# Kernel optimization log

Measured on AMD Instinct MI355X. Metric: run time of the kernel, lower is better.

The kernel has to match this reference:

```python
import jax, jax.numpy as jnp
import numpy as np

# ---- static config (matches init_kwargs) ----
N_NODES = 100_000; N_GRAPHS = 100; NPG = 1000; GRID = 32  # ceil(sqrt(1000))
N_EDGES = 1_600_000
IN_DIM = 64; POS_DIM = 16; HID = 16; HEADS = 4; HD = HID * HEADS  # 64
OUT_DIM = 10; DIV_WEIGHT = 0.1; BN_EPS = 1e-5; NEG_SLOPE = 0.2


def _segment_softmax(e, dst, n):
    emax = jax.ops.segment_max(e, dst, num_segments=n)
    p = jnp.exp(e - emax[dst])
    denom = jax.ops.segment_sum(p, dst, num_segments=n)
    return p / (denom[dst] + 1e-16)


def _gat(x, src, dst, n, W, a_src, a_dst, extra=None):
    """GATv1-style conv: per-head linear, additive attention, segment softmax over dst."""
    H, D = a_src.shape
    h = (x @ W).reshape(n, H, D)          # [N,H,D]
    s = (h * a_src).sum(-1)               # [N,H]
    d = (h * a_dst).sum(-1)               # [N,H]
    e = s[src] + d[dst]
    if extra is not None:
        e = e + extra                     # positional attention bias [E,H]
    e = jax.nn.leaky_relu(e, NEG_SLOPE)
    alpha = _segment_softmax(e, dst, n)   # [E,H]
    out = jax.ops.segment_sum(alpha[:, :, None] * h[src], dst, num_segments=n)
    return out.reshape(n, H * D)


def _div_loss(W):
    # head-diversity / orthogonality regularizer on per-head weight slices
    in_dim = W.shape[0]
    Wh = W.reshape(in_dim, HEADS, HID).transpose(1, 0, 2).reshape(HEADS, -1)
    Wn = Wh / (jnp.linalg.norm(Wh, axis=-1, keepdims=True) + 1e-12)
    G = Wn @ Wn.T
    off = G - jnp.eye(HEADS, dtype=W.dtype)
    return DIV_WEIGHT * (off ** 2).sum() / (HEADS * (HEADS - 1))


def _grid_pos(n, dtype):
    # normalized grid positions per graph (equal-size graphs of NPG nodes)
    i = jnp.arange(n) % NPG
    return jnp.stack([(i // GRID) / (GRID - 1), (i % GRID) / (GRID - 1)], -1).astype(dtype)


def _forward(x, edge_index, batch,
             pe_W, pe_b,
             l0_pW, l0_pas, l0_pad, l0_posW, l0_posb, l0_dW, l0_das, l0_dad, l0_fW, l0_fb, l0_g, l0_b,
             l1_pW, l1_pas, l1_pad, l1_posW, l1_posb, l1_dW, l1_das, l1_dad, l1_fW, l1_fb, l1_g, l1_b,
             res_W, res_b, task_W, task_b):
    n = x.shape[0]
    src, dst = edge_index[0], edge_index[1]
    pos = _grid_pos(n, x.dtype)
    rel = pos[dst] - pos[src]             # [E,2]
    h = jnp.concatenate([x, pos @ pe_W + pe_b], -1)  # positional encoding concat [N,80]

    def layer(h_in, pW, pas, pad, posW, posb, dW, das, dad, fW, fb, g, b):
        pos_out = _gat(h_in, src, dst, n, pW, pas, pad, extra=rel @ posW + posb)
        div_out = _gat(h_in, src, dst, n, dW, das, dad)
        fused = jnp.concatenate([pos_out, div_out], -1) @ fW + fb
        mu = fused.mean(0)
        var = fused.var(0)
        bn = (fused - mu) / jnp.sqrt(var + BN_EPS) * g + b
        return jax.nn.elu(bn), _div_loss(dW)

    h1, dl0 = layer(h, l0_pW, l0_pas, l0_pad, l0_posW, l0_posb, l0_dW, l0_das, l0_dad, l0_fW, l0_fb, l0_g, l0_b)
    h2, dl1 = layer(h1, l1_pW, l1_pas, l1_pad, l1_posW, l1_posb, l1_dW, l1_das, l1_dad, l1_fW, l1_fb, l1_g, l1_b)
    h2 = h2 + (h1 @ res_W + res_b)        # residual on layer >0

    pooled = jax.ops.segment_sum(h2, batch, num_segments=N_GRAPHS) / NPG  # mean pool
    task = pooled @ task_W + task_b       # [N_GRAPHS, OUT_DIM]
    return task, dl0 + dl1


def setup_inputs() -> dict:
    key = jax.random.key(0)
    keys = iter(jax.random.split(key, 64))
    nk = lambda: next(keys)
    w = lambda shape: jax.random.normal(nk(), shape, jnp.float32) * 0.05
    x = jax.random.normal(nk(), (N_NODES, IN_DIM), jnp.float32)
    gid = jnp.repeat(jnp.arange(N_GRAPHS), N_EDGES // N_GRAPHS)
    src = gid * NPG + jax.random.randint(nk(), (N_EDGES,), 0, NPG)
    dst = gid * NPG + jax.random.randint(nk(), (N_EDGES,), 0, NPG)
    edge_index = jnp.stack([src, dst]).astype(jnp.int32)
    batch = jnp.repeat(jnp.arange(N_GRAPHS), NPG).astype(jnp.int32)
    IN0 = IN_DIM + POS_DIM
    inp = dict(x=x, edge_index=edge_index, batch=batch,
               pe_W=w((2, POS_DIM)), pe_b=jnp.zeros((POS_DIM,), jnp.float32))
    for pref, din in (('l0', IN0), ('l1', HD)):
        inp[pref + '_pW'] = w((din, HD)); inp[pref + '_pas'] = w((HEADS, HID)); inp[pref + '_pad'] = w((HEADS, HID))
        inp[pref + '_posW'] = w((2, HEADS)); inp[pref + '_posb'] = jnp.zeros((HEADS,), jnp.float32)
        inp[pref + '_dW'] = w((din, HD)); inp[pref + '_das'] = w((HEADS, HID)); inp[pref + '_dad'] = w((HEADS, HID))
        inp[pref + '_fW'] = w((2 * HD, HD)); inp[pref + '_fb'] = jnp.zeros((HD,), jnp.float32)
        inp[pref + '_g'] = jnp.ones((HD,), jnp.float32); inp[pref + '_b'] = jnp.zeros((HD,), jnp.float32)
    inp['res_W'] = w((HD, HD)); inp['res_b'] = jnp.zeros((HD,), jnp.float32)
    inp['task_W'] = w((HD, OUT_DIM)); inp['task_b'] = jnp.zeros((OUT_DIM,), jnp.float32)
    return inp


def reference(x, edge_index, batch,
              pe_W, pe_b,
              l0_pW, l0_pas, l0_pad, l0_posW, l0_posb, l0_dW, l0_das, l0_dad, l0_fW, l0_fb, l0_g, l0_b,
              l1_pW, l1_pas, l1_pad, l1_posW, l1_posb, l1_dW, l1_das, l1_dad, l1_fW, l1_fb, l1_g, l1_b,
              res_W, res_b, task_W, task_b):
    return _forward(x, edge_index, batch, pe_W, pe_b,
                    l0_pW, l0_pas, l0_pad, l0_posW, l0_posb, l0_dW, l0_das, l0_dad, l0_fW, l0_fb, l0_g, l0_b,
                    l1_pW, l1_pas, l1_pad, l1_posW, l1_posb, l1_dW, l1_das, l1_dad, l1_fW, l1_fb, l1_g, l1_b,
                    res_W, res_b, task_W, task_b)
```

## Files before the change

### kernel.cpp

```cpp
#include <hip/hip_runtime.h>
#include <math.h>

#define N_NODES   100000
#define N_GRAPHS  100
#define NPG       1000
#define N_EDGES   1600000
#define EPG       16000
#define HID       16
#define HEADS     4
#define HD        64
#define OUT_DIM   10
#define BN_EPS    1e-5f
#define NEG_SLOPE 0.2f

#define LDA 68
#define BF_BLOCKS 782

static const size_t OFF_SPART = 0;
static const size_t OFF_PEWS  = 7000000;
static const size_t OFF_STAT1 = 7001000;
static const size_t OFF_WFRAG = 7010000;
static const size_t OFF_WF2   = 7020000;
static const size_t OFF_POOL  = 7100000;
static const size_t OFF_HL    = 8000000;
static const size_t OFF_CAT   = 20800000;
static const size_t OFF_F0    = 33600000;
static const size_t OFF_F1    = 40000000;
static const size_t OFF_SPSP  = 46400000;
static const size_t OFF_SPSD  = 46800000;
static const size_t OFF_DPD   = 47200000;
static const size_t OFF_STATS = 48000000;
static const size_t OFF_CSR   = 48000128;
static const size_t OFF_SRT   = 48100144;

__device__ inline unsigned bf_pack(float x, float y) {
    unsigned ux = __float_as_uint(x);
    unsigned uy = __float_as_uint(y);
    ux = (ux + 0x7FFFu + ((ux >> 16) & 1u)) >> 16;
    uy = ((uy + 0x7FFFu + ((uy >> 16) & 1u)) >> 16) << 16;
    return ux | uy;
}
__device__ inline float bf_lo(unsigned u) { return __uint_as_float(u << 16); }
__device__ inline float bf_hi(unsigned u) { return __uint_as_float(u & 0xFFFF0000u); }

typedef __attribute__((ext_vector_type(8))) short bf16x8;
typedef __attribute__((ext_vector_type(4))) float f32x4;

__device__ inline bf16x8 frag_from(unsigned a, unsigned b, unsigned c, unsigned d) {
    uint4 u{a, b, c, d};
    return *reinterpret_cast<bf16x8*>(&u);
}

__global__ __launch_bounds__(1024) void sort_edges(const int* __restrict__ ei,
                                                   int* __restrict__ csr_off,
                                                   int* __restrict__ sorted_src) {
    __shared__ int hist[1024];
    __shared__ int scan[1024];
    const int g = blockIdx.x;
    const int t = threadIdx.x;
    const int* src = ei;
    const int* dst = ei + N_EDGES;
    const int e0 = g * EPG;
    const int nbase = g * NPG;

    hist[t] = 0;
    __syncthreads();
    for (int i = t; i < EPG; i += 1024) {
        int d = dst[e0 + i] - nbase;
        atomicAdd(&hist[d], 1);
    }
    __syncthreads();
    scan[t] = hist[t];
    __syncthreads();
    for (int off = 1; off < 1024; off <<= 1) {
        int v = (t >= off) ? scan[t - off] : 0;
        __syncthreads();
        scan[t] += v;
        __syncthreads();
    }
    int excl = scan[t] - hist[t];
    if (t < NPG) csr_off[nbase + t] = e0 + excl;
    if (g == 0 && t == 0) csr_off[N_NODES] = N_EDGES;
    __syncthreads();
    hist[t] = excl;
    __syncthreads();
    for (int i = t; i < EPG; i += 1024) {
        int s = src[e0 + i];
        int d = dst[e0 + i] - nbase;
        int slot = atomicAdd(&hist[d], 1);
        sorted_src[e0 + slot] = s;
    }
}

__global__ __launch_bounds__(256) void prep_all(const float* __restrict__ peW, const float* __restrict__ peb,
                                                const float* __restrict__ pW0, const float* __restrict__ dW0,
                                                const float* __restrict__ pW1, const float* __restrict__ dW1,
                                                const float* __restrict__ fW0, const float* __restrict__ fW1,
                                                float* __restrict__ pe,
                                                uint4* __restrict__ wfA,
                                                uint4* __restrict__ wfD,
                                                float* __restrict__ pool2,
                                                float* __restrict__ stats0,
                                                float* __restrict__ stats1) {
    const int t = threadIdx.x;
    const int b = blockIdx.x;
    if (b == 0) {
        if (t < 128) {
            int r = t >> 6, c = t & 63;
            float sp = 0.f, sd = 0.f;
            for (int m = 0; m < 16; ++m) {
                sp += peW[r * 16 + m] * pW0[(64 + m) * 64 + c];
                sd += peW[r * 16 + m] * dW0[(64 + m) * 64 + c];
            }
            pe[r * 64 + c] = sp;
            pe[192 + r * 64 + c] = sd;
        } else if (t < 192) {
            int c = t & 63;
            float sp = 0.f, sd = 0.f;
            for (int m = 0; m < 16; ++m) {
                sp += peb[m] * pW0[(64 + m) * 64 + c];
                sd += peb[m] * dW0[(64 + m) * 64 + c];
            }
            pe[128 + c] = sp;
            pe[320 + c] = sd;
        }
    } else if (b == 1) {
        for (int i = t; i < 2 * 4 * 4 * 64; i += 256) {
            const int lane  = i & 63;
            const int ct    = (i >> 6) & 3;
            const int kk    = (i >> 8) & 3;
            const int layer = i >> 10;
            const float* W = layer ? fW1 : fW0;
            const int col = ct * 16 + (lane & 15);
            const int kb  = kk * 32 + (lane >> 4) * 8;
            uint4 u;
            u.x = bf_pack(W[(kb + 0) * 64 + col], W[(kb + 1) * 64 + col]);
            u.y = bf_pack(W[(kb + 2) * 64 + col], W[(kb + 3) * 64 + col]);
            u.z = bf_pack(W[(kb + 4) * 64 + col], W[(kb + 5) * 64 + col]);
            u.w = bf_pack(W[(kb + 6) * 64 + col], W[(kb + 7) * 64 + col]);
            wfA[i] = u;
        }
    } else if (b == 2) {
        for (int i = t; i < 2048; i += 256) {
            const int lane  = i & 63;
            const int ct    = (i >> 6) & 3;
            const int kk    = (i >> 8) & 1;
            const int mat   = (i >> 9) & 1;
            const int layer = i >> 10;
            const float* W = layer ? (mat ? dW1 : pW1) : (mat ? dW0 : pW0);
            const int col = ct * 16 + (lane & 15);
            const int kb  = kk * 32 + (lane >> 4) * 8;
            uint4 u;
            u.x = bf_pack(W[(kb + 0) * 64 + col], W[(kb + 1) * 64 + col]);
            u.y = bf_pack(W[(kb + 2) * 64 + col], W[(kb + 3) * 64 + col]);
            u.z = bf_pack(W[(kb + 4) * 64 + col], W[(kb + 5) * 64 + col]);
            u.w = bf_pack(W[(kb + 6) * 64 + col], W[(kb + 7) * 64 + col]);
            wfD[i] = u;
        }
    } else {
        for (int i = t; i < 2 * N_GRAPHS * 64; i += 256) pool2[i] = 0.f;
        if (t < 128) { stats0[t] = 0.f; stats1[t] = 0.f; }
    }
}

__global__ __launch_bounds__(128) void reduce_stats(const float* __restrict__ part,
                                                    float* __restrict__ stats, int nb) {
    const int c = threadIdx.x;
    const int per = (nb + gridDim.x - 1) / gridDim.x;
    const int b0 = blockIdx.x * per;
    int b1 = b0 + per; if (b1 > nb) b1 = nb;
    float s = 0.f;
    for (int b = b0; b < b1; ++b) s += part[(size_t)b * 128 + c];
    atomicAdd(&stats[c], s);
}

template <bool PE, bool BN>
__global__ __launch_bounds__(256) void gemm_dual_mfma(const float* __restrict__ A,
                                                      const unsigned* __restrict__ wf2,
                                                      const float* __restrict__ pe,
                                                      const float* __restrict__ pas,
                                                      const float* __restrict__ pad_,
                                                      const float* __restrict__ das,
                                                      const float* __restrict__ dad,
                                                      const float* __restrict__ posW,
                                                      const float* __restrict__ posb,
                                                      const float* __restrict__ stats,
                                                      const float* __restrict__ gamma,
                                                      const float* __restrict__ beta,
                                                      float* __restrict__ poolF,
                                                      unsigned* __restrict__ hl,
                                                      float* __restrict__ sps_p,
                                                      float* __restrict__ sps_d,
                                                      float2* __restrict__ dpd) {
    __shared__ float sD[4 * 2 * 16 * LDA];
    const int t = threadIdx.x;
    const int w = t >> 6, lane = t & 63;
    const int cidx = lane & 15, khi = lane >> 4;
    const int node0 = blockIdx.x * 64;

    bf16x8 wf[2][2][4];
#pragma unroll
    for (int mat = 0; mat < 2; ++mat)
#pragma unroll
        for (int kk = 0; kk < 2; ++kk)
#pragma unroll
            for (int ct = 0; ct < 4; ++ct)
                wf[mat][kk][ct] = *reinterpret_cast<const bf16x8*>(
                    wf2 + (size_t)((((mat * 2 + kk) * 4 + ct) * 64) + lane) * 4);

    const int node0w = node0 + w * 16;
    int gn = node0w + cidx; if (gn > N_NODES - 1) gn = N_NODES - 1;
    const float* ar = A + (size_t)gn * 64;
    bf16x8 ah[2], al[2];
#pragma unroll
    for (int kk = 0; kk < 2; ++kk) {
        const int k0 = kk * 32 + khi * 8;
        float4 f0 = *reinterpret_cast<const float4*>(ar + k0);
        float4 f1 = *reinterpret_cast<const float4*>(ar + k0 + 4);
        if (BN) {
            const float invN = 1.0f / (float)N_NODES;
            float4 sa = *reinterpret_cast<const float4*>(&stats[k0]);
            float4 sb = *reinterpret_cast<const float4*>(&stats[k0 + 4]);
            float4 qa = *reinterpret_cast<const float4*>(&stats[64 + k0]);
            float4 qb = *reinterpret_cast<const float4*>(&stats[64 + k0 + 4]);
            float4 ga = *reinterpret_cast<const float4*>(&gamma[k0]);
            float4 gb = *reinterpret_cast<const float4*>(&gamma[k0 + 4]);
            float4 ba = *reinterpret_cast<const float4*>(&beta[k0]);
            float4 bb = *reinterpret_cast<const float4*>(&beta[k0 + 4]);
            float sc[8], sh[8];
            float ss[8] = {sa.x, sa.y, sa.z, sa.w, sb.x, sb.y, sb.z, sb.w};
            float qq[8] = {qa.x, qa.y, qa.z, qa.w, qb.x, qb.y, qb.z, qb.w};
            float gg[8] = {ga.x, ga.y, ga.z, ga.w, gb.x, gb.y, gb.z, gb.w};
            float bt[8] = {ba.x, ba.y, ba.z, ba.w, bb.x, bb.y, bb.z, bb.w};
#pragma unroll
            for (int i = 0; i < 8; ++i) {
                float mu = ss[i] * invN;
                float var = qq[i] * invN - mu * mu;
                float iv = rsqrtf(var + BN_EPS);
                sc[i] = iv * gg[i];
                sh[i] = bt[i] - mu * sc[i];
            }
            auto ap = [&](float v, int i) {
                float r = fmaf(v, sc[i], sh[i]);
                return r > 0.f ? r : (__expf(r) - 1.f);
            };
            f0.x = ap(f0.x, 0); f0.y = ap(f0.y, 1); f0.z = ap(f0.z, 2); f0.w = ap(f0.w, 3);
            f1.x = ap(f1.x, 4); f1.y = ap(f1.y, 5); f1.z = ap(f1.z, 6); f1.w = ap(f1.w, 7);
            if (node0w < N_NODES) {
                const int node_l = node0w + cidx;
                const bool okn = node_l < N_NODES;
                const int gl = node_l / NPG;
                const int g0 = node0w / NPG;
                int lastn = node0w + 15; if (lastn > N_NODES - 1) lastn = N_NODES - 1;
                const int g1 = lastn / NPG;
                float p8[8] = {f0.x, f0.y, f0.z, f0.w, f1.x, f1.y, f1.z, f1.w};
                {
                    const bool m = okn && (gl == g0);
#pragma unroll
                    for (int i = 0; i < 8; ++i) {
                        float tv = m ? p8[i] : 0.f;
                        tv += __shfl_xor(tv, 1); tv += __shfl_xor(tv, 2);
                        tv += __shfl_xor(tv, 4); tv += __shfl_xor(tv, 8);
                        if (cidx == 0) atomicAdd(&poolF[g0 * 64 + k0 + i], tv);
                    }
                }
                if (g1 != g0) {
                    const bool m = okn && (gl == g1);
#pragma unroll
                    for (int i = 0; i < 8; ++i) {
                        float tv = m ? p8[i] : 0.f;
                        tv += __shfl_xor(tv, 1); tv += __shfl_xor(tv, 2);
                        tv += __shfl_xor(tv, 4); tv += __shfl_xor(tv, 8);
                        if (cidx == 0) atomicAdd(&poolF[g1 * 64 + k0 + i], tv);
                    }
                }
            }
        }
        unsigned h0 = bf_pack(f0.x, f0.y), h1 = bf_pack(f0.z, f0.w);
        unsigned h2 = bf_pack(f1.x, f1.y), h3 = bf_pack(f1.z, f1.w);
        unsigned l0 = bf_pack(f0.x - bf_lo(h0), f0.y - bf_hi(h0));
        unsigned l1 = bf_pack(f0.z - bf_lo(h1), f0.w - bf_hi(h1));
        unsigned l2 = bf_pack(f1.x - bf_lo(h2), f1.y - bf_hi(h2));
        unsigned l3 = bf_pack(f1.z - bf_lo(h3), f1.w - bf_hi(h3));
        ah[kk] = frag_from(h0, h1, h2, h3);
        al[kk] = frag_from(l0, l1, l2, l3);
    }

    f32x4 ap4[4], ad4[4];
#pragma unroll
    for (int ct = 0; ct < 4; ++ct) { ap4[ct] = 0.f; ad4[ct] = 0.f; }
#pragma unroll
    for (int ct = 0; ct < 4; ++ct) {
        ap4[ct] = __builtin_amdgcn_mfma_f32_16x16x32_bf16(ah[0], wf[0][0][ct], ap4[ct], 0, 0, 0);
        ap4[ct] = __builtin_amdgcn_mfma_f32_16x16x32_bf16(ah[1], wf[0][1][ct], ap4[ct], 0, 0, 0);
        ap4[ct] = __builtin_amdgcn_mfma_f32_16x16x32_bf16(al[0], wf[0][0][ct], ap4[ct], 0, 0, 0);
        ap4[ct] = __builtin_amdgcn_mfma_f32_16x16x32_bf16(al[1], wf[0][1][ct], ap4[ct], 0, 0, 0);
        ad4[ct] = __builtin_amdgcn_mfma_f32_16x16x32_bf16(ah[0], wf[1][0][ct], ad4[ct], 0, 0, 0);
        ad4[ct] = __builtin_amdgcn_mfma_f32_16x16x32_bf16(ah[1], wf[1][1][ct], ad4[ct], 0, 0, 0);
        ad4[ct] = __builtin_amdgcn_mfma_f32_16x16x32_bf16(al[0], wf[1][0][ct], ad4[ct], 0, 0, 0);
        ad4[ct] = __builtin_amdgcn_mfma_f32_16x16x32_bf16(al[1], wf[1][1][ct], ad4[ct], 0, 0, 0);
    }

    {
        float* base = sD + w * (2 * 16 * LDA);
#pragma unroll
        for (int ct = 0; ct < 4; ++ct)
#pragma unroll
            for (int q = 0; q < 4; ++q) {
                base[(khi * 4 + q) * LDA + ct * 16 + cidx]                 = ap4[ct][q];
                base[16 * LDA + (khi * 4 + q) * LDA + ct * 16 + cidx]      = ad4[ct][q];
            }
    }
    __syncthreads();

    const int tx = t & 15, ty = t >> 4;
    const int c4 = tx * 4;
    float4 accp[4], accd[4];
#pragma unroll
    for (int j = 0; j < 4; ++j) {
        const int n = ty * 4 + j;
        const float* bp = sD + (n >> 4) * (2 * 16 * LDA) + (n & 15) * LDA;
        accp[j] = *reinterpret_cast<const float4*>(bp + c4);
        accd[j] = *reinterpret_cast<const float4*>(bp + 16 * LDA + c4);
    }

    if (PE) {
        float4 pp0 = *reinterpret_cast<const float4*>(&pe[c4]);
        float4 pp1 = *reinterpret_cast<const float4*>(&pe[64 + c4]);
        float4 ppb = *reinterpret_cast<const float4*>(&pe[128 + c4]);
        float4 pd0 = *reinterpret_cast<const float4*>(&pe[192 + c4]);
        float4 pd1 = *reinterpret_cast<const float4*>(&pe[256 + c4]);
        float4 pdb = *reinterpret_cast<const float4*>(&pe[320 + c4]);
#pragma unroll
        for (int j = 0; j < 4; ++j) {
            int node = node0 + ty * 4 + j;
            int r = node % NPG;
            float px = (float)(r >> 5) * (1.0f / 31.0f);
            float py = (float)(r & 31) * (1.0f / 31.0f);
            accp[j].x += px * pp0.x + py * pp1.x + ppb.x;
            accp[j].y += px * pp0.y + py * pp1.y + ppb.y;
            accp[j].z += px * pp0.z + py * pp1.z + ppb.z;
            accp[j].w += px * pp0.w + py * pp1.w + ppb.w;
            accd[j].x += px * pd0.x + py * pd1.x + pdb.x;
            accd[j].y += px * pd0.y + py * pd1.y + pdb.y;
            accd[j].z += px * pd0.z + py * pd1.z + pdb.z;
            accd[j].w += px * pd0.w + py * pd1.w + pdb.w;
        }
    }

    float4 pasv = *reinterpret_cast<const float4*>(&pas[c4]);
    float4 padv = *reinterpret_cast<const float4*>(&pad_[c4]);
    float4 dasv = *reinterpret_cast<const float4*>(&das[c4]);
    float4 dadv = *reinterpret_cast<const float4*>(&dad[c4]);
    const int h = tx >> 2;
    const float pw0 = posW[h], pw1 = posW[4 + h], pb = posb[h];
    const int cu = tx * 2;
#pragma unroll
    for (int j = 0; j < 4; ++j) {
        const int node = node0 + ty * 4 + j;
        float vps = accp[j].x * pasv.x + accp[j].y * pasv.y + accp[j].z * pasv.z + accp[j].w * pasv.w;
        float vpd = accp[j].x * padv.x + accp[j].y * padv.y + accp[j].z * padv.z + accp[j].w * padv.w;
        float vds = accd[j].x * dasv.x + accd[j].y * dasv.y + accd[j].z * dasv.z + accd[j].w * dasv.w;
        float vdd = accd[j].x * dadv.x + accd[j].y * dadv.y + accd[j].z * dadv.z + accd[j].w * dadv.w;
        vps += __shfl_xor(vps, 1); vps += __shfl_xor(vps, 2);
        vpd += __shfl_xor(vpd, 1); vpd += __shfl_xor(vpd, 2);
        vds += __shfl_xor(vds, 1); vds += __shfl_xor(vds, 2);
        vdd += __shfl_xor(vdd, 1); vdd += __shfl_xor(vdd, 2);
        if (node < N_NODES) {
            uint2 up, ud;
            up.x = bf_pack(accp[j].x, accp[j].y); up.y = bf_pack(accp[j].z, accp[j].w);
            ud.x = bf_pack(accd[j].x, accd[j].y); ud.y = bf_pack(accd[j].z, accd[j].w);
            *reinterpret_cast<uint2*>(&hl[(size_t)node * 64 + cu])      = up;
            *reinterpret_cast<uint2*>(&hl[(size_t)node * 64 + 32 + cu]) = ud;
            if ((tx & 3) == 0) {
                const int r = node % NPG;
                const float pxn = (float)(r >> 5) * (1.0f / 31.0f);
                const float pyn = (float)(r & 31) * (1.0f / 31.0f);
                const float posdot = pxn * pw0 + pyn * pw1;
                sps_p[node * 4 + h] = vps - posdot;
                sps_d[node * 4 + h] = vds;
                dpd[node * 4 + h] = float2{vpd + posdot + pb, vdd};
            }
        }
    }
}

__global__ __launch_bounds__(256) void gemm_mfma_bf(const unsigned* __restrict__ A,
                                                    const unsigned* __restrict__ wfrag,
                                                    const float* __restrict__ bias,
                                                    float* __restrict__ out,
                                                    float* __restrict__ spart) {
    __shared__ float red[512];
    const int t = threadIdx.x;
    const int lane = t & 63;
    const int cidx = lane & 15;
    const int khi  = lane >> 4;

    bf16x8 wf[4][4];
#pragma unroll
    for (int kk = 0; kk < 4; ++kk)
#pragma unroll
        for (int ct = 0; ct < 4; ++ct)
            wf[kk][ct] = *reinterpret_cast<const bf16x8*>(wfrag + (size_t)((kk * 4 + ct) * 64 + lane) * 4);

    float bias_r[4];
#pragma unroll
    for (int ct = 0; ct < 4; ++ct) bias_r[ct] = bias[ct * 16 + cidx];

    float ls[4] = {0.f, 0.f, 0.f, 0.f};
    float lq[4] = {0.f, 0.f, 0.f, 0.f};

    const int NW  = gridDim.x << 2;
    const int wid = (blockIdx.x << 2) + (t >> 6);
    for (int tile = wid; tile < N_NODES / 16; tile += NW) {
        const int node0 = tile << 4;
        const unsigned* arow = A + (size_t)(node0 + cidx) * 64 + khi * 4;
        bf16x8 a0 = *reinterpret_cast<const bf16x8*>(arow);
        bf16x8 a1 = *reinterpret_cast<const bf16x8*>(arow + 16);
        bf16x8 a2 = *reinterpret_cast<const bf16x8*>(arow + 32);
        bf16x8 a3 = *reinterpret_cast<const bf16x8*>(arow + 48);

        f32x4 acc[4];
#pragma unroll
        for (int ct = 0; ct < 4; ++ct) acc[ct] = 0.f;
#pragma unroll
        for (int ct = 0; ct < 4; ++ct) {
            acc[ct] = __builtin_amdgcn_mfma_f32_16x16x32_bf16(a0, wf[0][ct], acc[ct], 0, 0, 0);
            acc[ct] = __builtin_amdgcn_mfma_f32_16x16x32_bf16(a1, wf[1][ct], acc[ct], 0, 0, 0);
            acc[ct] = __builtin_amdgcn_mfma_f32_16x16x32_bf16(a2, wf[2][ct], acc[ct], 0, 0, 0);
            acc[ct] = __builtin_amdgcn_mfma_f32_16x16x32_bf16(a3, wf[3][ct], acc[ct], 0, 0, 0);
        }

        const int nbase = node0 + (khi << 2);
#pragma unroll
        for (int ct = 0; ct < 4; ++ct) {
#pragma unroll
            for (int q = 0; q < 4; ++q) {
                float v = acc[ct][q] + bias_r[ct];
                out[(size_t)(nbase + q) * 64 + ct * 16 + cidx] = v;
                ls[ct] += v;
                lq[ct] = fmaf(v, v, lq[ct]);
            }
        }
    }

#pragma unroll
    for (int ct = 0; ct < 4; ++ct) {
        ls[ct] += __shfl_xor(ls[ct], 16); ls[ct] += __shfl_xor(ls[ct], 32);
        lq[ct] += __shfl_xor(lq[ct], 16); lq[ct] += __shfl_xor(lq[ct], 32);
    }
    if (lane < 16) {
        const int w = t >> 6;
#pragma unroll
        for (int ct = 0; ct < 4; ++ct) {
            red[w * 64 + ct * 16 + lane]       = ls[ct];
            red[256 + w * 64 + ct * 16 + lane] = lq[ct];
        }
    }
    __syncthreads();
    if (t < 64) {
        float s  = red[t] + red[64 + t] + red[128 + t] + red[192 + t];
        float sq = red[256 + t] + red[320 + t] + red[384 + t] + red[448 + t];
        spart[(size_t)blockIdx.x * 128 + t]      = s;
        spart[(size_t)blockIdx.x * 128 + 64 + t] = sq;
    }
}

__global__ __launch_bounds__(256) void gat_fused(const unsigned* __restrict__ hl,
                                                 const float* __restrict__ sps_p,
                                                 const float* __restrict__ sps_d,
                                                 const float2* __restrict__ dpd,
                                                 const int* __restrict__ csr_off,
                                                 const int* __restrict__ sorted_src,
                                                 unsigned* __restrict__ gat_cat) {
    const int b = blockIdx.x;
    const int logical = (b & 7) * 3125 + (b >> 3);
    const int v = logical * 4 + (threadIdx.x >> 6);
    if (v >= N_NODES) return;
    const int lane = threadIdx.x & 63;
    const int j1 = lane >> 3;
    const int p1 = (lane >> 2) & 1;
    const int h1 = lane & 3;
    const int phneed = ((lane >> 5) << 2) | ((lane & 31) >> 3);

    const float* __restrict__ spl = p1 ? sps_d : sps_p;
    const float2 dv1 = dpd[(size_t)v * 4 + h1];
    const float dval1 = p1 ? dv1.y : dv1.x;

    const int beg = __builtin_amdgcn_readfirstlane(csr_off[v]);
    const int end = __builtin_amdgcn_readfirstlane(csr_off[v + 1]);

    float2 acc = {0.f, 0.f};
    float wpart = 0.f;
    int e = beg;
    const int nfull = (end - beg) >> 3;

    int sA = 0, sB = 0;
    float svA = 0.f, svB = 0.f;
    if (nfull >= 1) { sA = sorted_src[e + j1]; svA = spl[(size_t)sA * 4 + h1]; }
    if (nfull >= 2) { sB = sorted_src[e + 8 + j1]; }

    for (int k = 0; k < nfull; ++k, e += 8) {
        int sC = 0;
        if (k + 2 < nfull) sC = sorted_src[e + 16 + j1];
        if (k + 1 < nfull) svB = spl[(size_t)sB * 4 + h1];
        float elog = svA + dval1;
        elog = fmaxf(elog, NEG_SLOPE * elog);
        float w = __expf(elog);
        wpart += w;
#pragma unroll
        for (int jj = 0; jj < 8; ++jj) {
            int sj = __builtin_amdgcn_readlane(sA, jj * 8);
            float wj = __shfl(w, jj * 8 + phneed);
            unsigned u = hl[((size_t)sj << 6) + lane];
            acc.x = fmaf(wj, bf_lo(u), acc.x);
            acc.y = fmaf(wj, bf_hi(u), acc.y);
        }
        sA = sB; sB = sC; svA = svB;
    }

    if (e < end) {
        const int nj = end - e;
        int ee = e + j1; if (ee >= end) ee = end - 1;
        int s = sorted_src[ee];
        float sval = spl[(size_t)s * 4 + h1];
        float elog = sval + dval1;
        elog = fmaxf(elog, NEG_SLOPE * elog);
        float w = __expf(elog);
        if (j1 >= nj) w = 0.f;
        wpart += w;
        for (int jj = 0; jj < nj; ++jj) {
            int sj = __builtin_amdgcn_readlane(s, jj * 8);
            float wj = __shfl(w, jj * 8 + phneed);
            unsigned u = hl[((size_t)sj << 6) + lane];
            acc.x = fmaf(wj, bf_lo(u), acc.x);
            acc.y = fmaf(wj, bf_hi(u), acc.y);
        }
    }
    wpart += __shfl_xor(wpart, 8);
    wpart += __shfl_xor(wpart, 16);
    wpart += __shfl_xor(wpart, 32);
    const float wsum = __shfl(wpart, phneed);
    const float inv = 1.0f / (wsum + 1e-16f);
    gat_cat[(size_t)v * 64 + lane] = bf_pack(acc.x * inv, acc.y * inv);
}

template <bool WRITEF>
__global__ __launch_bounds__(256) void bn_elu(float* __restrict__ F, const float* __restrict__ stats,
                                              const float* __restrict__ gamma, const float* __restrict__ beta,
                                              float* __restrict__ pooled) {
    __shared__ float red[256];
    const int t = threadIdx.x;
    const int idx = blockIdx.x * 256 + t;
    const int c = t & 63;
    float mu = stats[c] * (1.0f / (float)N_NODES);
    float var = stats[64 + c] * (1.0f / (float)N_NODES) - mu * mu;
    float inv = rsqrtf(var + BN_EPS);
    float v = (F[idx] - mu) * inv * gamma[c] + beta[c];
    v = (v > 0.f) ? v : expm1f(v);
    if (WRITEF) F[idx] = v;
    red[t] = v;
    __syncthreads();
    if (t < 64) {
        float s = red[c] + red[64 + c] + red[128 + c] + red[192 + c];
        int g = (blockIdx.x * 4) / NPG;
        atomicAdd(&pooled[g * 64 + c], s);
    }
}

__global__ __launch_bounds__(64) void task_head(const float* __restrict__ pooled,
                                                const float* __restrict__ pooledF0,
                                                const float* __restrict__ resW,
                                                const float* __restrict__ resb,
                                                const float* __restrict__ taskW,
                                                const float* __restrict__ taskb,
                                                float* __restrict__ out) {
    const int g = blockIdx.x;
    const int c = threadIdx.x;
    float rc = 0.f;
    const float* pf = pooledF0 + g * 64;
    for (int k = 0; k < 64; ++k)
        rc = fmaf(pf[k], resW[k * 64 + c], rc);
    float p = (pooled[g * 64 + c] + rc) * (1.0f / (float)NPG) + resb[c];
#pragma unroll
    for (int o = 0; o < OUT_DIM; ++o) {
        float partial = p * taskW[c * OUT_DIM + o];
#pragma unroll
        for (int m = 1; m < 64; m <<= 1) partial += __shfl_xor(partial, m);
        if (c == 0) out[g * OUT_DIM + o] = partial + taskb[o];
    }
}

__global__ __launch_bounds__(256) void div_loss(const float* __restrict__ dW0,
                                                const float* __restrict__ dW1,
                                                float* __restrict__ out) {
    __shared__ float red[16][16];
    float total = 0.f;
    for (int layer = 0; layer < 2; ++layer) {
        const float* W = layer ? dW1 : dW0;
        const int din = layer ? 64 : 80;
        const int p = threadIdx.x & 15;
        const int s16 = threadIdx.x >> 4;
        const int i = p >> 2, j = p & 3;
        float acc = 0.f;
        const int Kk = din * 16;
        for (int kk = s16; kk < Kk; kk += 16) {
            int rrow = kk >> 4, cc = kk & 15;
            acc += W[rrow * 64 + i * 16 + cc] * W[rrow * 64 + j * 16 + cc];
        }
        red[p][s16] = acc;
        __syncthreads();
        if (threadIdx.x < 16) {
            float s = 0.f;
            for (int m = 0; m < 16; ++m) s += red[threadIdx.x][m];
            red[threadIdx.x][0] = s;
        }
        __syncthreads();
        if (threadIdx.x == 0) {
            float G[4][4], nrm[4];
            for (int a = 0; a < 4; ++a)
                for (int b = 0; b < 4; ++b) G[a][b] = red[a * 4 + b][0];
            for (int a = 0; a < 4; ++a) nrm[a] = sqrtf(G[a][a]) + 1e-12f;
            float l = 0.f;
            for (int a = 0; a < 4; ++a)
                for (int b = 0; b < 4; ++b) {
                    float gn = G[a][b] / (nrm[a] * nrm[b]);
                    float off = gn - (a == b ? 1.f : 0.f);
                    l += off * off;
                }
            total += 0.1f * l / 12.f;
        }
        __syncthreads();
    }
    if (threadIdx.x == 0) *out = total;
}

extern "C" void kernel_launch(void* const* d_in, const int* in_sizes, int n_in,
                              void* d_out, int out_size, void* d_ws, size_t ws_size,
                              hipStream_t stream) {
    const float* x      = (const float*)d_in[0];
    const int*   ei     = (const int*)d_in[1];
    const float* peW    = (const float*)d_in[3];
    const float* peb    = (const float*)d_in[4];

    const float* l_pW[2]   = {(const float*)d_in[5],  (const float*)d_in[17]};
    const float* l_pas[2]  = {(const float*)d_in[6],  (const float*)d_in[18]};
    const float* l_pad[2]  = {(const float*)d_in[7],  (const float*)d_in[19]};
    const float* l_posW[2] = {(const float*)d_in[8],  (const float*)d_in[20]};
    const float* l_posb[2] = {(const float*)d_in[9],  (const float*)d_in[21]};
    const float* l_dW[2]   = {(const float*)d_in[10], (const float*)d_in[22]};
    const float* l_das[2]  = {(const float*)d_in[11], (const float*)d_in[23]};
    const float* l_dad[2]  = {(const float*)d_in[12], (const float*)d_in[24]};
    const float* l_fW[2]   = {(const float*)d_in[13], (const float*)d_in[25]};
    const float* l_fb[2]   = {(const float*)d_in[14], (const float*)d_in[26]};
    const float* l_g[2]    = {(const float*)d_in[15], (const float*)d_in[27]};
    const float* l_b[2]    = {(const float*)d_in[16], (const float*)d_in[28]};
    const float* res_W  = (const float*)d_in[29];
    const float* res_b  = (const float*)d_in[30];
    const float* task_W = (const float*)d_in[31];
    const float* task_b = (const float*)d_in[32];

    float* ws = (float*)d_ws;
    float* spart   = ws + OFF_SPART;
    float* pe_ws   = ws + OFF_PEWS;
    float* stats1  = ws + OFF_STAT1;
    float* wfrag   = ws + OFF_WFRAG;
    float* wfrag2  = ws + OFF_WF2;
    float* pooled  = ws + OFF_POOL;
    float* pooledF0= ws + OFF_POOL + 6400;
    unsigned* hl   = (unsigned*)(ws + OFF_HL);
    unsigned* cat_bf = (unsigned*)(ws + OFF_CAT);
    float* F0      = ws + OFF_F0;
    float* F1      = ws + OFF_F1;
    float* sps_p   = ws + OFF_SPSP;
    float* sps_d   = ws + OFF_SPSD;
    float2* dpd    = (float2*)(ws + OFF_DPD);
    float* stats0  = ws + OFF_STATS;
    int*   csr_off    = (int*)(ws + OFF_CSR);
    int*   sorted_src = (int*)(ws + OFF_SRT);
    float* out = (float*)d_out;

    const int NODE_BLOCKS = (N_NODES + 3) / 4;
    const int GEMM_BLOCKS = (N_NODES + 63) / 64;
    const int BN_BLOCKS   = N_NODES * 64 / 256;

    sort_edges<<<N_GRAPHS, 1024, 0, stream>>>(ei, csr_off, sorted_src);
    prep_all<<<4, 256, 0, stream>>>(peW, peb, l_pW[0], l_dW[0], l_pW[1], l_dW[1],
                                    l_fW[0], l_fW[1], pe_ws,
                                    (uint4*)wfrag, (uint4*)wfrag2,
                                    pooled, stats0, stats1);

    gemm_dual_mfma<true, false><<<GEMM_BLOCKS, 256, 0, stream>>>(x, (const unsigned*)wfrag2, pe_ws,
        l_pas[0], l_pad[0], l_das[0], l_dad[0], l_posW[0], l_posb[0],
        stats0, l_g[0], l_b[0], pooledF0,
        hl, sps_p, sps_d, dpd);
    gat_fused<<<NODE_BLOCKS, 256, 0, stream>>>(hl, sps_p, sps_d, dpd, csr_off, sorted_src, cat_bf);
    gemm_mfma_bf<<<BF_BLOCKS, 256, 0, stream>>>(cat_bf, (const unsigned*)wfrag,
                                                l_fb[0], F0, spart);
    reduce_stats<<<16, 128, 0, stream>>>(spart, stats0, BF_BLOCKS);

    gemm_dual_mfma<false, true><<<GEMM_BLOCKS, 256, 0, stream>>>(F0, (const unsigned*)wfrag2 + 4096, pe_ws,
        l_pas[1], l_pad[1], l_das[1], l_dad[1], l_posW[1], l_posb[1],
        stats0, l_g[0], l_b[0], pooledF0,
        hl, sps_p, sps_d, dpd);
    gat_fused<<<NODE_BLOCKS, 256, 0, stream>>>(hl, sps_p, sps_d, dpd, csr_off, sorted_src, cat_bf);
    gemm_mfma_bf<<<BF_BLOCKS, 256, 0, stream>>>(cat_bf, (const unsigned*)wfrag + 4096,
                                                l_fb[1], F1, spart);
    reduce_stats<<<16, 128, 0, stream>>>(spart, stats1, BF_BLOCKS);
    bn_elu<false><<<BN_BLOCKS, 256, 0, stream>>>(F1, stats1, l_g[1], l_b[1], pooled);

    task_head<<<N_GRAPHS, 64, 0, stream>>>(pooled, pooledF0, res_W, res_b,
                                           task_W, task_b, out);
    div_loss<<<1, 256, 0, stream>>>(l_dW[0], l_dW[1], out + 1000);
}
```

Before: 457.3 us.

## Merge sort and prep kernels, batch gather loads, pool BN per graph chunk

Merges the edge-sort and weight-prep launches into one kernel that uses extra blocks for the prep work, removing one launch. The GAT aggregation loop is unrolled by hand so all eight neighbor-row gathers are issued before the FMAs, which raises memory-level parallelism. The final BN+ELU+pool kernel changes from 25,000 tiny blocks each doing one atomic to 500 blocks that each reduce 200 nodes, cutting atomic and launch overhead. In exchange, each pooling block does more serial work and there is less parallelism.

```diff
diff --git a/kernel.cpp b/kernel.cpp
--- a/kernel.cpp
+++ b/kernel.cpp
@@ -15,6 +15,8 @@
 
 #define LDA 68
 #define BF_BLOCKS 782
+#define PB_PER_GRAPH 5
+#define PB_NODES 200
 
 static const size_t OFF_SPART = 0;
 static const size_t OFF_PEWS  = 7000000;
@@ -51,13 +53,87 @@
     return *reinterpret_cast<bf16x8*>(&u);
 }
 
-__global__ __launch_bounds__(1024) void sort_edges(const int* __restrict__ ei,
-                                                   int* __restrict__ csr_off,
-                                                   int* __restrict__ sorted_src) {
+__global__ __launch_bounds__(1024) void sort_prep(const int* __restrict__ ei,
+                                                  int* __restrict__ csr_off,
+                                                  int* __restrict__ sorted_src,
+                                                  const float* __restrict__ peW, const float* __restrict__ peb,
+                                                  const float* __restrict__ pW0, const float* __restrict__ dW0,
+                                                  const float* __restrict__ pW1, const float* __restrict__ dW1,
+                                                  const float* __restrict__ fW0, const float* __restrict__ fW1,
+                                                  float* __restrict__ pe,
+                                                  uint4* __restrict__ wfA,
+                                                  uint4* __restrict__ wfD,
+                                                  float* __restrict__ pool2,
+                                                  float* __restrict__ stats0,
+                                                  float* __restrict__ stats1) {
+    const int g = blockIdx.x;
+    const int t = threadIdx.x;
+    if (g >= N_GRAPHS) {
+        const int b = g - N_GRAPHS;
+        if (b == 0) {
+            if (t < 128) {
+                int r = t >> 6, c = t & 63;
+                float sp = 0.f, sd = 0.f;
+                for (int m = 0; m < 16; ++m) {
+                    sp += peW[r * 16 + m] * pW0[(64 + m) * 64 + c];
+                    sd += peW[r * 16 + m] * dW0[(64 + m) * 64 + c];
+                }
+                pe[r * 64 + c] = sp;
+                pe[192 + r * 64 + c] = sd;
+            } else if (t < 192) {
+                int c = t & 63;
+                float sp = 0.f, sd = 0.f;
+                for (int m = 0; m < 16; ++m) {
+                    sp += peb[m] * pW0[(64 + m) * 64 + c];
+                    sd += peb[m] * dW0[(64 + m) * 64 + c];
+                }
+                pe[128 + c] = sp;
+                pe[320 + c] = sd;
+            }
+        } else if (b == 1) {
+            if (t < 256)
+            for (int i = t; i < 2 * 4 * 4 * 64; i += 256) {
+                const int lane  = i & 63;
+                const int ct    = (i >> 6) & 3;
+                const int kk    = (i >> 8) & 3;
+                const int layer = i >> 10;
+                const float* W = layer ? fW1 : fW0;
+                const int col = ct * 16 + (lane & 15);
+                const int kb  = kk * 32 + (lane >> 4) * 8;
+                uint4 u;
+                u.x = bf_pack(W[(kb + 0) * 64 + col], W[(kb + 1) * 64 + col]);
+                u.y = bf_pack(W[(kb + 2) * 64 + col], W[(kb + 3) * 64 + col]);
+                u.z = bf_pack(W[(kb + 4) * 64 + col], W[(kb + 5) * 64 + col]);
+                u.w = bf_pack(W[(kb + 6) * 64 + col], W[(kb + 7) * 64 + col]);
+                wfA[i] = u;
+            }
+        } else if (b == 2) {
+            if (t < 256)
+            for (int i = t; i < 2048; i += 256) {
+                const int lane  = i & 63;
+                const int ct    = (i >> 6) & 3;
+                const int kk    = (i >> 8) & 1;
+                const int mat   = (i >> 9) & 1;
+                const int layer = i >> 10;
+                const float* W = layer ? (mat ? dW1 : pW1) : (mat ? dW0 : pW0);
+                const int col = ct * 16 + (lane & 15);
+                const int kb  = kk * 32 + (lane >> 4) * 8;
+                uint4 u;
+                u.x = bf_pack(W[(kb + 0) * 64 + col], W[(kb + 1) * 64 + col]);
+                u.y = bf_pack(W[(kb + 2) * 64 + col], W[(kb + 3) * 64 + col]);
+                u.z = bf_pack(W[(kb + 4) * 64 + col], W[(kb + 5) * 64 + col]);
+                u.w = bf_pack(W[(kb + 6) * 64 + col], W[(kb + 7) * 64 + col]);
+                wfD[i] = u;
+            }
+        } else {
+            for (int i = t; i < 2 * N_GRAPHS * 64; i += 1024) pool2[i] = 0.f;
+            if (t < 128) { stats0[t] = 0.f; stats1[t] = 0.f; }
+        }
+        return;
+    }
+
     __shared__ int hist[1024];
     __shared__ int scan[1024];
-    const int g = blockIdx.x;
-    const int t = threadIdx.x;
     const int* src = ei;
     const int* dst = ei + N_EDGES;
     const int e0 = g * EPG;
@@ -89,77 +165,6 @@
         int d = dst[e0 + i] - nbase;
         int slot = atomicAdd(&hist[d], 1);
         sorted_src[e0 + slot] = s;
-    }
-}
-
-__global__ __launch_bounds__(256) void prep_all(const float* __restrict__ peW, const float* __restrict__ peb,
-                                                const float* __restrict__ pW0, const float* __restrict__ dW0,
-                                                const float* __restrict__ pW1, const float* __restrict__ dW1,
-                                                const float* __restrict__ fW0, const float* __restrict__ fW1,
-                                                float* __restrict__ pe,
-                                                uint4* __restrict__ wfA,
-                                                uint4* __restrict__ wfD,
-                                                float* __restrict__ pool2,
-                                                float* __restrict__ stats0,
-                                                float* __restrict__ stats1) {
-    const int t = threadIdx.x;
-    const int b = blockIdx.x;
-    if (b == 0) {
-        if (t < 128) {
-            int r = t >> 6, c = t & 63;
-            float sp = 0.f, sd = 0.f;
-            for (int m = 0; m < 16; ++m) {
-                sp += peW[r * 16 + m] * pW0[(64 + m) * 64 + c];
-                sd += peW[r * 16 + m] * dW0[(64 + m) * 64 + c];
-            }
-            pe[r * 64 + c] = sp;
-            pe[192 + r * 64 + c] = sd;
-        } else if (t < 192) {
-            int c = t & 63;
-            float sp = 0.f, sd = 0.f;
-            for (int m = 0; m < 16; ++m) {
-                sp += peb[m] * pW0[(64 + m) * 64 + c];
-                sd += peb[m] * dW0[(64 + m) * 64 + c];
-            }
-            pe[128 + c] = sp;
-            pe[320 + c] = sd;
-        }
-    } else if (b == 1) {
-        for (int i = t; i < 2 * 4 * 4 * 64; i += 256) {
-            const int lane  = i & 63;
-            const int ct    = (i >> 6) & 3;
-            const int kk    = (i >> 8) & 3;
-            const int layer = i >> 10;
-            const float* W = layer ? fW1 : fW0;
-            const int col = ct * 16 + (lane & 15);
-            const int kb  = kk * 32 + (lane >> 4) * 8;
-            uint4 u;
-            u.x = bf_pack(W[(kb + 0) * 64 + col], W[(kb + 1) * 64 + col]);
-            u.y = bf_pack(W[(kb + 2) * 64 + col], W[(kb + 3) * 64 + col]);
-            u.z = bf_pack(W[(kb + 4) * 64 + col], W[(kb + 5) * 64 + col]);
-            u.w = bf_pack(W[(kb + 6) * 64 + col], W[(kb + 7) * 64 + col]);
-            wfA[i] = u;
-        }
-    } else if (b == 2) {
-        for (int i = t; i < 2048; i += 256) {
-            const int lane  = i & 63;
-            const int ct    = (i >> 6) & 3;
-            const int kk    = (i >> 8) & 1;
-            const int mat   = (i >> 9) & 1;
-            const int layer = i >> 10;
-            const float* W = layer ? (mat ? dW1 : pW1) : (mat ? dW0 : pW0);
-            const int col = ct * 16 + (lane & 15);
-            const int kb  = kk * 32 + (lane >> 4) * 8;
-            uint4 u;
-            u.x = bf_pack(W[(kb + 0) * 64 + col], W[(kb + 1) * 64 + col]);
-            u.y = bf_pack(W[(kb + 2) * 64 + col], W[(kb + 3) * 64 + col]);
-            u.z = bf_pack(W[(kb + 4) * 64 + col], W[(kb + 5) * 64 + col]);
-            u.w = bf_pack(W[(kb + 6) * 64 + col], W[(kb + 7) * 64 + col]);
-            wfD[i] = u;
-        }
-    } else {
-        for (int i = t; i < 2 * N_GRAPHS * 64; i += 256) pool2[i] = 0.f;
-        if (t < 128) { stats0[t] = 0.f; stats1[t] = 0.f; }
     }
 }
 
@@ -508,14 +513,38 @@
         elog = fmaxf(elog, NEG_SLOPE * elog);
         float w = __expf(elog);
         wpart += w;
-#pragma unroll
-        for (int jj = 0; jj < 8; ++jj) {
-            int sj = __builtin_amdgcn_readlane(sA, jj * 8);
-            float wj = __shfl(w, jj * 8 + phneed);
-            unsigned u = hl[((size_t)sj << 6) + lane];
-            acc.x = fmaf(wj, bf_lo(u), acc.x);
-            acc.y = fmaf(wj, bf_hi(u), acc.y);
-        }
+        int sj0 = __builtin_amdgcn_readlane(sA, 0);
+        int sj1 = __builtin_amdgcn_readlane(sA, 8);
+        int sj2 = __builtin_amdgcn_readlane(sA, 16);
+        int sj3 = __builtin_amdgcn_readlane(sA, 24);
+        int sj4 = __builtin_amdgcn_readlane(sA, 32);
+        int sj5 = __builtin_amdgcn_readlane(sA, 40);
+        int sj6 = __builtin_amdgcn_readlane(sA, 48);
+        int sj7 = __builtin_amdgcn_readlane(sA, 56);
+        float wj0 = __shfl(w, 0 + phneed);
+        float wj1 = __shfl(w, 8 + phneed);
+        float wj2 = __shfl(w, 16 + phneed);
+        float wj3 = __shfl(w, 24 + phneed);
+        float wj4 = __shfl(w, 32 + phneed);
+        float wj5 = __shfl(w, 40 + phneed);
+        float wj6 = __shfl(w, 48 + phneed);
+        float wj7 = __shfl(w, 56 + phneed);
+        unsigned u0 = hl[((size_t)sj0 << 6) + lane];
+        unsigned u1 = hl[((size_t)sj1 << 6) + lane];
+        unsigned u2 = hl[((size_t)sj2 << 6) + lane];
+        unsigned u3 = hl[((size_t)sj3 << 6) + lane];
+        unsigned u4 = hl[((size_t)sj4 << 6) + lane];
+        unsigned u5 = hl[((size_t)sj5 << 6) + lane];
+        unsigned u6 = hl[((size_t)sj6 << 6) + lane];
+        unsigned u7 = hl[((size_t)sj7 << 6) + lane];
+        acc.x = fmaf(wj0, bf_lo(u0), acc.x); acc.y = fmaf(wj0, bf_hi(u0), acc.y);
+        acc.x = fmaf(wj1, bf_lo(u1), acc.x); acc.y = fmaf(wj1, bf_hi(u1), acc.y);
+        acc.x = fmaf(wj2, bf_lo(u2), acc.x); acc.y = fmaf(wj2, bf_hi(u2), acc.y);
+        acc.x = fmaf(wj3, bf_lo(u3), acc.x); acc.y = fmaf(wj3, bf_hi(u3), acc.y);
+        acc.x = fmaf(wj4, bf_lo(u4), acc.x); acc.y = fmaf(wj4, bf_hi(u4), acc.y);
+        acc.x = fmaf(wj5, bf_lo(u5), acc.x); acc.y = fmaf(wj5, bf_hi(u5), acc.y);
+        acc.x = fmaf(wj6, bf_lo(u6), acc.x); acc.y = fmaf(wj6, bf_hi(u6), acc.y);
+        acc.x = fmaf(wj7, bf_lo(u7), acc.x); acc.y = fmaf(wj7, bf_hi(u7), acc.y);
         sA = sB; sB = sC; svA = svB;
     }
 
@@ -545,27 +574,30 @@
     gat_cat[(size_t)v * 64 + lane] = bf_pack(acc.x * inv, acc.y * inv);
 }
 
-template <bool WRITEF>
-__global__ __launch_bounds__(256) void bn_elu(float* __restrict__ F, const float* __restrict__ stats,
-                                              const float* __restrict__ gamma, const float* __restrict__ beta,
-                                              float* __restrict__ pooled) {
+__global__ __launch_bounds__(256) void pool_bn(const float* __restrict__ F, const float* __restrict__ stats,
+                                               const float* __restrict__ gamma, const float* __restrict__ beta,
+                                               float* __restrict__ pooled) {
     __shared__ float red[256];
+    const int b = blockIdx.x;
+    const int g = b / PB_PER_GRAPH;
+    const int n0 = g * NPG + (b % PB_PER_GRAPH) * PB_NODES;
     const int t = threadIdx.x;
-    const int idx = blockIdx.x * 256 + t;
-    const int c = t & 63;
-    float mu = stats[c] * (1.0f / (float)N_NODES);
-    float var = stats[64 + c] * (1.0f / (float)N_NODES) - mu * mu;
-    float inv = rsqrtf(var + BN_EPS);
-    float v = (F[idx] - mu) * inv * gamma[c] + beta[c];
-    v = (v > 0.f) ? v : expm1f(v);
-    if (WRITEF) F[idx] = v;
-    red[t] = v;
+    const int c = t & 63, rg = t >> 6;
+    const float mu = stats[c] * (1.0f / (float)N_NODES);
+    const float var = stats[64 + c] * (1.0f / (float)N_NODES) - mu * mu;
+    const float iv = rsqrtf(var + BN_EPS);
+    const float sc = iv * gamma[c];
+    const float sh = beta[c] - mu * sc;
+    float s = 0.f;
+    for (int i = rg; i < PB_NODES; i += 4) {
+        float v = fmaf(F[(size_t)(n0 + i) * 64 + c], sc, sh);
+        v = (v > 0.f) ? v : expm1f(v);
+        s += v;
+    }
+    red[t] = s;
     __syncthreads();
-    if (t < 64) {
-        float s = red[c] + red[64 + c] + red[128 + c] + red[192 + c];
-        int g = (blockIdx.x * 4) / NPG;
-        atomicAdd(&pooled[g * 64 + c], s);
-    }
+    if (t < 64)
+        atomicAdd(&pooled[g * 64 + c], red[c] + red[64 + c] + red[128 + c] + red[192 + c]);
 }
 
 __global__ __launch_bounds__(64) void task_head(const float* __restrict__ pooled,
@@ -682,13 +714,11 @@
 
     const int NODE_BLOCKS = (N_NODES + 3) / 4;
     const int GEMM_BLOCKS = (N_NODES + 63) / 64;
-    const int BN_BLOCKS   = N_NODES * 64 / 256;
-
-    sort_edges<<<N_GRAPHS, 1024, 0, stream>>>(ei, csr_off, sorted_src);
-    prep_all<<<4, 256, 0, stream>>>(peW, peb, l_pW[0], l_dW[0], l_pW[1], l_dW[1],
-                                    l_fW[0], l_fW[1], pe_ws,
-                                    (uint4*)wfrag, (uint4*)wfrag2,
-                                    pooled, stats0, stats1);
+    const int PB_BLOCKS   = N_GRAPHS * PB_PER_GRAPH;
+
+    sort_prep<<<N_GRAPHS + 4, 1024, 0, stream>>>(ei, csr_off, sorted_src,
+        peW, peb, l_pW[0], l_dW[0], l_pW[1], l_dW[1], l_fW[0], l_fW[1],
+        pe_ws, (uint4*)wfrag, (uint4*)wfrag2, pooled, stats0, stats1);
 
     gemm_dual_mfma<true, false><<<GEMM_BLOCKS, 256, 0, stream>>>(x, (const unsigned*)wfrag2, pe_ws,
         l_pas[0], l_pad[0], l_das[0], l_dad[0], l_posW[0], l_posb[0],
@@ -707,7 +737,7 @@
     gemm_mfma_bf<<<BF_BLOCKS, 256, 0, stream>>>(cat_bf, (const unsigned*)wfrag + 4096,
                                                 l_fb[1], F1, spart);
     reduce_stats<<<16, 128, 0, stream>>>(spart, stats1, BF_BLOCKS);
-    bn_elu<false><<<BN_BLOCKS, 256, 0, stream>>>(F1, stats1, l_g[1], l_b[1], pooled);
+    pool_bn<<<PB_BLOCKS, 256, 0, stream>>>(F1, stats1, l_g[1], l_b[1], pooled);
 
     task_head<<<N_GRAPHS, 64, 0, stream>>>(pooled, pooledF0, res_W, res_b,
                                            task_W, task_b, out);
```

After: 443.2 us, median of 2. -3.1%, faster.
